# Kernel tuning notes

Measured on AMD Instinct MI355X. Metric: run time of the kernel, lower is better.

The kernel has to match this reference:

```python
import jax, jax.numpy as jnp
import numpy as np

N, M, D = 8192, 8192, 512

def setup_inputs() -> dict:
    key = jax.random.key(0)
    ks = jax.random.split(key, 8)
    s = 1.0 / np.sqrt(D)
    return {
        "x": jax.random.normal(ks[0], (N, D), jnp.float32),
        "domain_x": jax.random.normal(ks[1], (M, D), jnp.float32),
        "Wq": jax.random.normal(ks[2], (D, D), jnp.float32) * s,
        "bq": jax.random.normal(ks[3], (D,), jnp.float32) * s,
        "Wk": jax.random.normal(ks[4], (D, D), jnp.float32) * s,
        "bk": jax.random.normal(ks[5], (D,), jnp.float32) * s,
        "Wv": jax.random.normal(ks[6], (D, D), jnp.float32) * s,
        "bv": jax.random.normal(ks[7], (D,), jnp.float32) * s,
    }

def reference(x, domain_x, Wq, bq, Wk, bk, Wv, bv):
    # torch Linear: y = x @ W^T + b
    q = x @ Wq.T + bq            # [N, D]
    k = domain_x @ Wk.T + bk     # [M, D]
    v = domain_x @ Wv.T + bv     # [M, D]
    scale = jnp.sqrt(jnp.asarray(k.shape[-1], q.dtype))
    scores = q @ k.T             # [N, M]
    attn = jax.nn.softmax(scores / scale, axis=-1)
    return attn @ v              # [N, D]
```

## Files before the change

### kernel.cpp

```cpp
#include <hip/hip_runtime.h>
#include <stdint.h>


#define DEV __device__ __forceinline__

typedef short short8 __attribute__((ext_vector_type(8)));
typedef float floatx4 __attribute__((ext_vector_type(4)));
typedef unsigned int uintx4 __attribute__((ext_vector_type(4)));
typedef unsigned short ushortx4 __attribute__((ext_vector_type(4)));

constexpr int NN = 8192;
constexpr int MM = 8192;
constexpr int DD = 512;
constexpr float SCALE2 = 0.0637587160f;
constexpr float DEFER_THR = 6.0f;

#define NEG_INF (-__builtin_inff())

#if defined(__has_builtin)
#if __has_builtin(__builtin_amdgcn_exp2f)
#define EXP2F(x) __builtin_amdgcn_exp2f(x)
#else
#define EXP2F(x) exp2f(x)
#endif
#else
#define EXP2F(x) exp2f(x)
#endif

DEV unsigned short f2bf(float f) {
  unsigned u = __builtin_bit_cast(unsigned, f);
  return (unsigned short)((u + 0x7FFFu + ((u >> 16) & 1u)) >> 16);
}
DEV float bf2f(unsigned short h) {
  unsigned u = ((unsigned)h) << 16;
  return __builtin_bit_cast(float, u);
}

template <int CTRL>
DEV float dpp_rot(float x) {
  int xi = __builtin_bit_cast(int, x);
  return __builtin_bit_cast(float,
      __builtin_amdgcn_update_dpp(xi, xi, CTRL, 0xf, 0xf, false));
}
DEV float row_max16(float x) {
  x = fmaxf(x, dpp_rot<0x121>(x));
  x = fmaxf(x, dpp_rot<0x122>(x));
  x = fmaxf(x, dpp_rot<0x124>(x));
  x = fmaxf(x, dpp_rot<0x128>(x));
  return x;
}
DEV float row_sum16(float x) {
  x += dpp_rot<0x121>(x);
  x += dpp_rot<0x122>(x);
  x += dpp_rot<0x124>(x);
  x += dpp_rot<0x128>(x);
  return x;
}

DEV short8 ld_s8(const void* p) {
  short8 v; __builtin_memcpy(&v, __builtin_assume_aligned(p, 16), 16); return v;
}
DEV uintx4 ld_u4(const void* p) {
  uintx4 v; __builtin_memcpy(&v, __builtin_assume_aligned(p, 16), 16); return v;
}
DEV void st_u4(void* p, uintx4 v) {
  __builtin_memcpy(__builtin_assume_aligned(p, 16), &v, 16);
}
DEV void st_us4(void* p, ushortx4 v) {
  __builtin_memcpy(__builtin_assume_aligned(p, 8), &v, 8);
}
DEV float4 ld_f4(const void* p) {
  float4 v; __builtin_memcpy(&v, __builtin_assume_aligned(p, 16), 16); return v;
}

DEV void async_lds16(const void* g, const void* l) {
  __builtin_amdgcn_global_load_lds(
      (const __attribute__((address_space(1))) unsigned int*)g,
      (__attribute__((address_space(3))) unsigned int*)l, 16, 0, 0);
}

__global__ void prep_w(const float* __restrict__ Wq, const float* __restrict__ Wk,
                       const float* __restrict__ Wv, unsigned short* __restrict__ Wb) {
  const int z = blockIdx.z;
  const float* src = (z == 0) ? Wq : (z == 1) ? Wk : Wv;
  unsigned short* dst = Wb + (size_t)z * DD * DD;
  size_t idx = ((size_t)blockIdx.x * 256 + threadIdx.x) * 8;
  float4 a = ld_f4(src + idx);
  float4 b = ld_f4(src + idx + 4);
  ushortx4 lo = {f2bf(a.x), f2bf(a.y), f2bf(a.z), f2bf(a.w)};
  ushortx4 hi = {f2bf(b.x), f2bf(b.y), f2bf(b.z), f2bf(b.w)};
  st_us4(dst + idx, lo);
  st_us4(dst + idx + 4, hi);
}

__global__ __launch_bounds__(256, 2)
void qkv_proj(const float* __restrict__ x, const float* __restrict__ dx,
              const unsigned short* __restrict__ Wb,
              const float* __restrict__ bq, const float* __restrict__ bk,
              const float* __restrict__ bv,
              unsigned short* __restrict__ Qb, unsigned short* __restrict__ Kb,
              unsigned short* __restrict__ VTb) {
  const int z = blockIdx.z;
  const float* A = (z == 0) ? x : dx;
  const unsigned short* W = Wb + (size_t)z * DD * DD;
  const float* bias = (z == 0) ? bq : (z == 1) ? bk : bv;

  const int r0 = blockIdx.x * 64;
  const int c0 = blockIdx.y * 256;
  const int tid = threadIdx.x;
  const int lane = tid & 63;
  const int wave = tid >> 6;
  const int lr = lane & 15;
  const int quad = lane >> 4;

  __shared__ __align__(16) unsigned short As[64 * 64];
  __shared__ __align__(16) unsigned short Ws[256 * 64];

  floatx4 o[16];
#pragma unroll
  for (int i = 0; i < 16; ++i) o[i] = {0.f, 0.f, 0.f, 0.f};

  for (int k0 = 0; k0 < DD; k0 += 64) {
#pragma unroll
    for (int i = 0; i < 4; ++i) {
      int idx = i * 256 + tid;
      int r = idx >> 4, c4 = idx & 15;
      float4 v = ld_f4(A + (size_t)(r0 + r) * DD + k0 + c4 * 4);
      ushortx4 pk = {f2bf(v.x), f2bf(v.y), f2bf(v.z), f2bf(v.w)};
      st_us4(&As[r * 64 + (((c4 >> 1) ^ (r & 7)) * 8) + (c4 & 1) * 4], pk);
    }
#pragma unroll
    for (int i = 0; i < 8; ++i) {
      int idx = i * 256 + tid;
      int r = idx >> 3, c = idx & 7;
      uintx4 v = ld_u4(W + (size_t)(c0 + r) * DD + k0 + c * 8);
      st_u4(&Ws[r * 64 + ((c ^ (r & 7)) * 8)], v);
    }
    __syncthreads();

    short8 a[2];
#pragma unroll
    for (int ks = 0; ks < 2; ++ks)
      a[ks] = ld_s8(&As[(wave * 16 + lr) * 64 + (((ks * 4 + quad) ^ (lr & 7)) * 8)]);
#pragma unroll
    for (int ct = 0; ct < 16; ++ct) {
#pragma unroll
      for (int ks = 0; ks < 2; ++ks) {
        short8 b = ld_s8(&Ws[(ct * 16 + lr) * 64 + (((ks * 4 + quad) ^ (lr & 7)) * 8)]);
        o[ct] = __builtin_amdgcn_mfma_f32_16x16x32_bf16(a[ks], b, o[ct], 0, 0, 0);
      }
    }
    __syncthreads();
  }

#pragma unroll
  for (int ct = 0; ct < 16; ++ct) {
    int col = c0 + ct * 16 + lr;
    float bv_ = bias[col];
    int rowb = r0 + wave * 16 + quad * 4;
    if (z == 2) {
      ushortx4 pk = {f2bf(o[ct][0] + bv_), f2bf(o[ct][1] + bv_),
                     f2bf(o[ct][2] + bv_), f2bf(o[ct][3] + bv_)};
      st_us4(VTb + (size_t)col * MM + rowb, pk);
    } else {
      unsigned short* Outp = (z == 0) ? Qb : Kb;
      float sc = (z == 0) ? SCALE2 : 1.f;
#pragma unroll
      for (int r = 0; r < 4; ++r)
        Outp[(size_t)(rowb + r) * DD + col] = f2bf((o[ct][r] + bv_) * sc);
    }
  }
}

template <int SPLITS_, int LOG2S_>
__global__ __launch_bounds__(256, 2)
void flash_attn(const unsigned short* __restrict__ Qb,
                const unsigned short* __restrict__ Kb,
                const unsigned short* __restrict__ VTb,
                unsigned short* __restrict__ Opart,
                float* __restrict__ Mpart, float* __restrict__ Lpart) {
  constexpr int MT = MM / SPLITS_;
  constexpr int ITERS = MT / 64;
  const int lin = blockIdx.x;
  const int split = lin & (SPLITS_ - 1);
  const int n0 = (lin >> LOG2S_) * 64;
  const int m_begin = split * MT;

  const int tid = threadIdx.x;
  const int lane = tid & 63;
  const int wave = tid >> 6;
  const int lr = lane & 15;
  const int quad = lane >> 4;

  __shared__ __align__(16) unsigned short sKV[33280];
  __shared__ __align__(16) unsigned short sP[64 * 64];
  __shared__ float sAlpha[64];
  __shared__ int sNeed;

  if (tid == 0) sNeed = 0;

  short8 qf[16];
  {
    const unsigned short* qptr = Qb + (size_t)(n0 + wave * 16 + lr) * DD + quad * 8;
#pragma unroll
    for (int ks = 0; ks < 16; ++ks) qf[ks] = ld_s8(qptr + ks * 32);
  }

  const int vrb = lane >> 3;
  const int vcb = ((lane & 7) ^ vrb) * 8;
  const unsigned short* vsrc0 = VTb + (size_t)(wave * 128 + vrb) * MM + vcb;
  unsigned short* vdst0 = &sKV[wave * 16 * 512];

  floatx4 o[32];
#pragma unroll
  for (int i = 0; i < 32; ++i) o[i] = {0.f, 0.f, 0.f, 0.f};
  float mrow[4] = {NEG_INF, NEG_INF, NEG_INF, NEG_INF};
  float lrow[4] = {0.f, 0.f, 0.f, 0.f};

  for (int it = 0; it < ITERS; ++it) {
    const int m0 = m_begin + it * 64;

#pragma unroll
    for (int i = 0; i < 16; ++i) {
      const int r = wave * 16 + i;
      async_lds16(Kb + (size_t)(m0 + r) * DD + lane * 8, &sKV[r * 520]);
    }
    __syncthreads();

    floatx4 s[4];
#pragma unroll
    for (int ct = 0; ct < 4; ++ct) s[ct] = {0.f, 0.f, 0.f, 0.f};
    __builtin_amdgcn_s_setprio(1);
#pragma unroll
    for (int ks = 0; ks < 16; ++ks) {
      const unsigned short* kb = &sKV[ks * 32 + quad * 8];
#pragma unroll
      for (int ct = 0; ct < 4; ++ct) {
        short8 b = ld_s8(kb + (ct * 16 + lr) * 520);
        s[ct] = __builtin_amdgcn_mfma_f32_16x16x32_bf16(qf[ks], b, s[ct], 0, 0, 0);
      }
    }
    __builtin_amdgcn_s_setprio(0);
    __syncthreads();

    {
      const unsigned short* src = vsrc0 + m0;
#pragma unroll
      for (int j = 0; j < 16; ++j)
        async_lds16(src + (size_t)j * 8 * MM, vdst0 + j * 512);
    }

    float alpha[4];
    bool anyresc = false;
#pragma unroll
    for (int r = 0; r < 4; ++r) {
      float mx = fmaxf(fmaxf(s[0][r], s[1][r]), fmaxf(s[2][r], s[3][r]));
      mx = row_max16(mx);
      float mnew = (mx > mrow[r] + DEFER_THR) ? mx : mrow[r];
      alpha[r] = EXP2F(mrow[r] - mnew);
      anyresc = anyresc || (mnew != mrow[r]);
      mrow[r] = mnew;
      float rs = 0.f;
#pragma unroll
      for (int ct = 0; ct < 4; ++ct) {
        float p = EXP2F(s[ct][r] - mnew);
        s[ct][r] = p;
        rs += p;
      }
      rs = row_sum16(rs);
      lrow[r] = lrow[r] * alpha[r] + rs;
    }
    if (__any(anyresc)) {
      if (lane == 0) sNeed = 1;
    }
    if (lr == 0) {
#pragma unroll
      for (int r = 0; r < 4; ++r) sAlpha[wave * 16 + quad * 4 + r] = alpha[r];
    }

#pragma unroll
    for (int ct = 0; ct < 4; ++ct)
#pragma unroll
      for (int r = 0; r < 4; ++r)
        sP[(wave * 16 + quad * 4 + r) * 64 +
           (((2 * ct + (lr >> 3)) ^ (2 * quad)) * 8) + (lr & 7)] = f2bf(s[ct][r]);

    __syncthreads();

    if (sNeed) {
      floatx4 af[4];
#pragma unroll
      for (int rt = 0; rt < 4; ++rt) {
        float4 t = ld_f4(&sAlpha[rt * 16 + quad * 4]);
        af[rt] = {t.x, t.y, t.z, t.w};
      }
#pragma unroll
      for (int rt = 0; rt < 4; ++rt)
#pragma unroll
        for (int ct = 0; ct < 8; ++ct)
#pragma unroll
          for (int r = 0; r < 4; ++r) o[rt * 8 + ct][r] *= af[rt][r];
    }

    __builtin_amdgcn_s_setprio(1);
#pragma unroll
    for (int ks = 0; ks < 2; ++ks) {
      short8 pa[4];
#pragma unroll
      for (int rt = 0; rt < 4; ++rt)
        pa[rt] = ld_s8(&sP[(rt * 16 + lr) * 64 +
                           (((4 * ks + quad) ^ (2 * ((lr >> 2) & 3))) * 8)]);
#pragma unroll
      for (int ct = 0; ct < 8; ++ct) {
        const int r = wave * 128 + ct * 16 + lr;
        short8 b = ld_s8(&sKV[r * 64 + (((ks * 4 + quad) ^ (lr & 7)) * 8)]);
#pragma unroll
        for (int rt = 0; rt < 4; ++rt)
          o[rt * 8 + ct] = __builtin_amdgcn_mfma_f32_16x16x32_bf16(pa[rt], b,
                                                                   o[rt * 8 + ct], 0, 0, 0);
      }
    }
    __builtin_amdgcn_s_setprio(0);
    __syncthreads();
    if (tid == 0) sNeed = 0;
  }

  unsigned short* op = Opart + (size_t)split * NN * DD;
#pragma unroll
  for (int rt = 0; rt < 4; ++rt)
#pragma unroll
    for (int ct = 0; ct < 8; ++ct) {
      int row = n0 + rt * 16 + quad * 4;
      int col = wave * 128 + ct * 16 + lr;
#pragma unroll
      for (int r = 0; r < 4; ++r)
        op[(size_t)(row + r) * DD + col] = f2bf(o[rt * 8 + ct][r]);
    }
  const int grow = n0 + wave * 16 + quad * 4;
  if (lr == 0) {
#pragma unroll
    for (int r = 0; r < 4; ++r) {
      Mpart[split * NN + grow + r] = mrow[r];
      Lpart[split * NN + grow + r] = lrow[r];
    }
  }
}

template <int SPLITS_>
__global__ void combine_kernel(const unsigned short* __restrict__ Op,
                               const float* __restrict__ Mp,
                               const float* __restrict__ Lp,
                               float* __restrict__ out) {
  constexpr size_t NDv = (size_t)NN * DD;
  size_t base = ((size_t)blockIdx.x * 256 + threadIdx.x) * 8;
  int n = (int)(base >> 9);
  float mv[SPLITS_];
  float ms = NEG_INF;
#pragma unroll
  for (int s = 0; s < SPLITS_; ++s) {
    mv[s] = Mp[s * NN + n];
    ms = fmaxf(ms, mv[s]);
  }
  float num[8];
#pragma unroll
  for (int j = 0; j < 8; ++j) num[j] = 0.f;
  float den = 0.f;
#pragma unroll
  for (int s = 0; s < SPLITS_; ++s) {
    float w = EXP2F(mv[s] - ms);
    den += w * Lp[s * NN + n];
    uintx4 u = ld_u4(Op + s * NDv + base);
#pragma unroll
    for (int j = 0; j < 4; ++j) {
      num[2 * j]     += w * bf2f((unsigned short)(u[j] & 0xffffu));
      num[2 * j + 1] += w * bf2f((unsigned short)(u[j] >> 16));
    }
  }
  float inv = 1.f / den;
  float4 o0 = {num[0] * inv, num[1] * inv, num[2] * inv, num[3] * inv};
  float4 o1 = {num[4] * inv, num[5] * inv, num[6] * inv, num[7] * inv};
  __builtin_memcpy(__builtin_assume_aligned(out + base, 16), &o0, 16);
  __builtin_memcpy(__builtin_assume_aligned(out + base + 4, 16), &o1, 16);
}

extern "C" void kernel_launch(void* const* d_in, const int* in_sizes, int n_in,
                              void* d_out, int out_size, void* d_ws, size_t ws_size,
                              hipStream_t stream) {
  const float* x  = (const float*)d_in[0];
  const float* dx = (const float*)d_in[1];
  const float* Wq = (const float*)d_in[2];
  const float* bq = (const float*)d_in[3];
  const float* Wk = (const float*)d_in[4];
  const float* bk = (const float*)d_in[5];
  const float* Wv = (const float*)d_in[6];
  const float* bv = (const float*)d_in[7];
  float* out = (float*)d_out;

  const size_t ND = (size_t)NN * DD;
  const size_t WBE = (size_t)3 * DD * DD;
  unsigned short* Qb  = (unsigned short*)d_ws;
  unsigned short* Kb  = Qb + ND;
  unsigned short* VTb = Kb + ND;
  unsigned short* Wb  = VTb + ND;
  unsigned short* Op  = Wb + WBE;

  auto bytes_for = [&](size_t S) {
    return (3 * ND + WBE + S * ND) * 2 + S * (size_t)NN * 8;
  };
  const int splits = (ws_size >= bytes_for(4)) ? 4 : 2;
  float* Mp = (float*)(Op + (size_t)splits * ND);
  float* Lp = Mp + (size_t)splits * NN;

  hipLaunchKernelGGL(prep_w, dim3(DD * DD / 2048, 1, 3), dim3(256), 0, stream,
                     Wq, Wk, Wv, Wb);
  hipLaunchKernelGGL(qkv_proj, dim3(NN / 64, 2, 3), dim3(256), 0, stream,
                     x, dx, Wb, bq, bk, bv, Qb, Kb, VTb);
  if (splits == 4) {
    hipLaunchKernelGGL((flash_attn<4, 2>), dim3(NN / 64 * 4), dim3(256), 0, stream,
                       Qb, Kb, VTb, Op, Mp, Lp);
    hipLaunchKernelGGL(combine_kernel<4>, dim3((unsigned)(ND / 2048)), dim3(256), 0, stream,
                       Op, Mp, Lp, out);
  } else {
    hipLaunchKernelGGL((flash_attn<2, 1>), dim3(NN / 64 * 2), dim3(256), 0, stream,
                       Qb, Kb, VTb, Op, Mp, Lp);
    hipLaunchKernelGGL(combine_kernel<2>, dim3((unsigned)(ND / 2048)), dim3(256), 0, stream,
                       Op, Mp, Lp, out);
  }
}
```

Measured before the change: 311.3 us.

## Use 128-row query tiles per 512-thread block with separate K/V buffers and K prefetch

```diff
diff --git a/kernel.cpp b/kernel.cpp
--- a/kernel.cpp
+++ b/kernel.cpp
@@ -173,7 +173,7 @@
 }
 
 template <int SPLITS_, int LOG2S_>
-__global__ __launch_bounds__(256, 2)
+__global__ __launch_bounds__(512, 2)
 void flash_attn(const unsigned short* __restrict__ Qb,
                 const unsigned short* __restrict__ Kb,
                 const unsigned short* __restrict__ VTb,
@@ -183,7 +183,7 @@
   constexpr int ITERS = MT / 64;
   const int lin = blockIdx.x;
   const int split = lin & (SPLITS_ - 1);
-  const int n0 = (lin >> LOG2S_) * 64;
+  const int n0 = (lin >> LOG2S_) * 128;
   const int m_begin = split * MT;
 
   const int tid = threadIdx.x;
@@ -191,10 +191,13 @@
   const int wave = tid >> 6;
   const int lr = lane & 15;
   const int quad = lane >> 4;
-
-  __shared__ __align__(16) unsigned short sKV[33280];
-  __shared__ __align__(16) unsigned short sP[64 * 64];
-  __shared__ float sAlpha[64];
+  const int wrow = wave & 1;
+  const int wcol = wave >> 1;
+
+  __shared__ __align__(16) unsigned short sK[64 * 520];
+  __shared__ __align__(16) unsigned short sVT[512 * 64];
+  __shared__ __align__(16) unsigned short sP[128 * 64];
+  __shared__ float sAlpha[128];
   __shared__ int sNeed;
 
   if (tid == 0) sNeed = 0;
@@ -208,8 +211,8 @@
 
   const int vrb = lane >> 3;
   const int vcb = ((lane & 7) ^ vrb) * 8;
-  const unsigned short* vsrc0 = VTb + (size_t)(wave * 128 + vrb) * MM + vcb;
-  unsigned short* vdst0 = &sKV[wave * 16 * 512];
+  const unsigned short* vsrc0 = VTb + (size_t)(wave * 64 + vrb) * MM + vcb;
+  unsigned short* vdst0 = &sVT[wave * 64 * 64];
 
   floatx4 o[32];
 #pragma unroll
@@ -217,15 +220,22 @@
   float mrow[4] = {NEG_INF, NEG_INF, NEG_INF, NEG_INF};
   float lrow[4] = {0.f, 0.f, 0.f, 0.f};
 
+#pragma unroll
+  for (int i = 0; i < 8; ++i) {
+    const int r = wave * 8 + i;
+    async_lds16(Kb + (size_t)(m_begin + r) * DD + lane * 8, &sK[r * 520]);
+  }
+  __syncthreads();
+
   for (int it = 0; it < ITERS; ++it) {
     const int m0 = m_begin + it * 64;
 
-#pragma unroll
-    for (int i = 0; i < 16; ++i) {
-      const int r = wave * 16 + i;
-      async_lds16(Kb + (size_t)(m0 + r) * DD + lane * 8, &sKV[r * 520]);
-    }
-    __syncthreads();
+    {
+      const unsigned short* src = vsrc0 + m0;
+#pragma unroll
+      for (int j = 0; j < 8; ++j)
+        async_lds16(src + (size_t)j * 8 * MM, vdst0 + j * 512);
+    }
 
     floatx4 s[4];
 #pragma unroll
@@ -233,7 +243,7 @@
     __builtin_amdgcn_s_setprio(1);
 #pragma unroll
     for (int ks = 0; ks < 16; ++ks) {
-      const unsigned short* kb = &sKV[ks * 32 + quad * 8];
+      const unsigned short* kb = &sK[ks * 32 + quad * 8];
 #pragma unroll
       for (int ct = 0; ct < 4; ++ct) {
         short8 b = ld_s8(kb + (ct * 16 + lr) * 520);
@@ -243,11 +253,12 @@
     __builtin_amdgcn_s_setprio(0);
     __syncthreads();
 
-    {
-      const unsigned short* src = vsrc0 + m0;
-#pragma unroll
-      for (int j = 0; j < 16; ++j)
-        async_lds16(src + (size_t)j * 8 * MM, vdst0 + j * 512);
+    if (it + 1 < ITERS) {
+#pragma unroll
+      for (int i = 0; i < 8; ++i) {
+        const int r = wave * 8 + i;
+        async_lds16(Kb + (size_t)(m0 + 64 + r) * DD + lane * 8, &sK[r * 520]);
+      }
     }
 
     float alpha[4];
@@ -288,18 +299,17 @@
     __syncthreads();
 
     if (sNeed) {
-      floatx4 af[4];
 #pragma unroll
       for (int rt = 0; rt < 4; ++rt) {
-        float4 t = ld_f4(&sAlpha[rt * 16 + quad * 4]);
-        af[rt] = {t.x, t.y, t.z, t.w};
-      }
-#pragma unroll
-      for (int rt = 0; rt < 4; ++rt)
-#pragma unroll
-        for (int ct = 0; ct < 8; ++ct)
-#pragma unroll
-          for (int r = 0; r < 4; ++r) o[rt * 8 + ct][r] *= af[rt][r];
+        float4 t = ld_f4(&sAlpha[wrow * 64 + rt * 16 + quad * 4]);
+#pragma unroll
+        for (int ct = 0; ct < 8; ++ct) {
+          o[rt * 8 + ct][0] *= t.x;
+          o[rt * 8 + ct][1] *= t.y;
+          o[rt * 8 + ct][2] *= t.z;
+          o[rt * 8 + ct][3] *= t.w;
+        }
+      }
     }
 
     __builtin_amdgcn_s_setprio(1);
@@ -308,12 +318,12 @@
       short8 pa[4];
 #pragma unroll
       for (int rt = 0; rt < 4; ++rt)
-        pa[rt] = ld_s8(&sP[(rt * 16 + lr) * 64 +
+        pa[rt] = ld_s8(&sP[(wrow * 64 + rt * 16 + lr) * 64 +
                            (((4 * ks + quad) ^ (2 * ((lr >> 2) & 3))) * 8)]);
 #pragma unroll
       for (int ct = 0; ct < 8; ++ct) {
-        const int r = wave * 128 + ct * 16 + lr;
-        short8 b = ld_s8(&sKV[r * 64 + (((ks * 4 + quad) ^ (lr & 7)) * 8)]);
+        const int r = wcol * 128 + ct * 16 + lr;
+        short8 b = ld_s8(&sVT[r * 64 + (((ks * 4 + quad) ^ (lr & 7)) * 8)]);
 #pragma unroll
         for (int rt = 0; rt < 4; ++rt)
           o[rt * 8 + ct] = __builtin_amdgcn_mfma_f32_16x16x32_bf16(pa[rt], b,
@@ -330,8 +340,8 @@
   for (int rt = 0; rt < 4; ++rt)
 #pragma unroll
     for (int ct = 0; ct < 8; ++ct) {
-      int row = n0 + rt * 16 + quad * 4;
-      int col = wave * 128 + ct * 16 + lr;
+      int row = n0 + wrow * 64 + rt * 16 + quad * 4;
+      int col = wcol * 128 + ct * 16 + lr;
 #pragma unroll
       for (int r = 0; r < 4; ++r)
         op[(size_t)(row + r) * DD + col] = f2bf(o[rt * 8 + ct][r]);
@@ -416,12 +426,12 @@
   hipLaunchKernelGGL(qkv_proj, dim3(NN / 64, 2, 3), dim3(256), 0, stream,
                      x, dx, Wb, bq, bk, bv, Qb, Kb, VTb);
   if (splits == 4) {
-    hipLaunchKernelGGL((flash_attn<4, 2>), dim3(NN / 64 * 4), dim3(256), 0, stream,
+    hipLaunchKernelGGL((flash_attn<4, 2>), dim3(NN / 128 * 4), dim3(512), 0, stream,
                        Qb, Kb, VTb, Op, Mp, Lp);
     hipLaunchKernelGGL(combine_kernel<4>, dim3((unsigned)(ND / 2048)), dim3(256), 0, stream,
                        Op, Mp, Lp, out);
   } else {
-    hipLaunchKernelGGL((flash_attn<2, 1>), dim3(NN / 64 * 2), dim3(256), 0, stream,
+    hipLaunchKernelGGL((flash_attn<2, 1>), dim3(NN / 128 * 2), dim3(512), 0, stream,
                        Qb, Kb, VTb, Op, Mp, Lp);
     hipLaunchKernelGGL(combine_kernel<2>, dim3((unsigned)(ND / 2048)), dim3(256), 0, stream,
                        Op, Mp, Lp, out);
```

Result: slower. 320.7 us (+3.0%).
